# Optimization experiments

Hardware: AMD Instinct MI355X
Metric: run time of the kernel (lower is better)

## Reference

```python
import jax, jax.numpy as jnp
import numpy as np

N, E = 50000, 800000
IN_F, OUT_F, H = 128, 128, 4
D = OUT_F // H  # head dim
NEG_SLOPE = 0.2
EPS = 1e-12


def setup_inputs() -> dict:
    key = jax.random.key(0)
    ks = jax.random.split(key, 10)
    s = 1.0 / np.sqrt(IN_F)
    return {
        "x": jax.random.normal(ks[0], (N, IN_F), jnp.float32),
        "W_src": jax.random.normal(ks[1], (IN_F, H * D), jnp.float32) * s,
        "b_src": jnp.zeros((H * D,), jnp.float32),
        "W_dst": jax.random.normal(ks[2], (IN_F, H * D), jnp.float32) * s,
        "b_dst": jnp.zeros((H * D,), jnp.float32),
        "attn": jax.random.normal(ks[3], (H, D), jnp.float32) * (1.0 / np.sqrt(D)),
        "out_bias": jnp.zeros((H * D,), jnp.float32),
        "ln_w": jnp.ones((OUT_F,), jnp.float32),
        "ln_b": jnp.zeros((OUT_F,), jnp.float32),
        "src": jax.random.randint(ks[4], (E,), 0, N, jnp.int32),
        "dst": jax.random.randint(ks[5], (E,), 0, N, jnp.int32),
    }


def reference(x, W_src, b_src, W_dst, b_dst, attn, out_bias, ln_w, ln_b, src, dst):
    n = x.shape[0]
    # GATv2Conv (share_weights=False): separate source/dest projections
    fs = (x @ W_src + b_src).reshape(n, H, D)  # [N,H,D]
    fd = (x @ W_dst + b_dst).reshape(n, H, D)
    # per-edge scores: e_ij = attn . leaky_relu(fs[u] + fd[v])
    e = jax.nn.leaky_relu(fs[src] + fd[dst], NEG_SLOPE)  # [E,H,D]
    logits = jnp.einsum("ehd,hd->eh", e, attn)  # [E,H]
    # edge softmax over incoming edges of each dst node
    m = jax.ops.segment_max(logits, dst, num_segments=n)  # [N,H]
    ex = jnp.exp(logits - m[dst])
    denom = jax.ops.segment_sum(ex, dst, num_segments=n)  # [N,H]
    alpha = ex / denom[dst]  # [E,H]
    # aggregate: sum_j alpha_ij * fs[j]
    msg = alpha[:, :, None] * fs[src]  # [E,H,D]
    rst = jax.ops.segment_sum(msg, dst, num_segments=n)  # [N,H,D]
    h = rst.reshape(n, H * D) + out_bias
    # LayerNorm (biased variance, eps inside sqrt)
    u = h.mean(-1, keepdims=True)
    s = jnp.mean((h - u) ** 2, -1, keepdims=True)
    h = (h - u) / jnp.sqrt(s + EPS)
    h = ln_w * h + ln_b
    # activation = elu; dropout p=0 -> identity
    return jax.nn.elu(h)
```

## Files before the change

### kernel.cpp

```cpp
#include <hip/hip_runtime.h>
#include <hip/hip_bf16.h>

constexpr int NF = 128;

using bf16x8 = __attribute__((ext_vector_type(8))) short;
using f32x4v = __attribute__((ext_vector_type(4))) float;

__device__ __forceinline__ unsigned short f2bs(float f) {
    return __builtin_bit_cast(unsigned short, __float2bfloat16(f));
}
__device__ __forceinline__ void unpack8(float4 raw, float* a) {
    unsigned u0 = __float_as_uint(raw.x);
    unsigned u1 = __float_as_uint(raw.y);
    unsigned u2 = __float_as_uint(raw.z);
    unsigned u3 = __float_as_uint(raw.w);
    a[0] = __uint_as_float(u0 << 16);
    a[1] = __uint_as_float(u0 & 0xffff0000u);
    a[2] = __uint_as_float(u1 << 16);
    a[3] = __uint_as_float(u1 & 0xffff0000u);
    a[4] = __uint_as_float(u2 << 16);
    a[5] = __uint_as_float(u2 & 0xffff0000u);
    a[6] = __uint_as_float(u3 << 16);
    a[7] = __uint_as_float(u3 & 0xffff0000u);
}

__global__ void GraphAttnLayer_70196945486348_kernel() {}

__global__ __launch_bounds__(256) void prep_kernel(
    const float* __restrict__ Wsrc, const float* __restrict__ Wdst,
    unsigned short* __restrict__ Wb2,
    int* __restrict__ state, int NSB)
{
    int i = blockIdx.x * 256 + threadIdx.x;
    if (i < NSB) state[i] = 0;
    if (i < 16 * 256) {
        int j = i >> 8;
        int t = i & 255;
        int wave = t >> 6;
        int lane = t & 63;
        int lm = lane & 15;
        int kq = (lane >> 4) * 8;
        int c = j >> 2, s = j & 3;
        int col = wave * 64 + c * 16 + lm;
        int ks = s * 32 + kq;
        bf16x8 frag;
#pragma unroll
        for (int m = 0; m < 8; ++m) {
            float v = (col < 128) ? Wsrc[(ks + m) * NF + col]
                                  : Wdst[(ks + m) * NF + (col - 128)];
            frag[m] = (short)f2bs(v);
        }
        *(bf16x8*)(Wb2 + (size_t)i * 8) = frag;
    }
}

__global__ __launch_bounds__(256) void gemm_hist_kernel(
    const float* __restrict__ x,
    const unsigned short* __restrict__ Wb2,
    const float* __restrict__ bsrc, const float* __restrict__ bdst,
    unsigned short* __restrict__ fs,
    float* __restrict__ fd,
    const int* __restrict__ dst,
    int* __restrict__ cntT,
    int N, int E, int C, int B)
{
    __shared__ int lh[256];
    __shared__ float xs[32][129];
    const int t = threadIdx.x;
    if (blockIdx.x < C) {
        lh[t] = 0;
        __syncthreads();
        int e0 = blockIdx.x * 4096;
#pragma unroll
        for (int j = 0; j < 16; ++j) {
            int e = e0 + j * 256 + t;
            if (e < E) atomicAdd(&lh[dst[e] >> 8], 1);
        }
        __syncthreads();
        if (t < B) cntT[t * C + blockIdx.x] = lh[t];
    }

    const int lane = t & 63;
    const int wave = t >> 6;
    const int m_base = blockIdx.x * 32;
    if (m_base >= N) return;
    const int lm = lane & 15;
    const int kq = (lane >> 4) * 8;

    bf16x8 bfrag[4][4];
    float bias[4];
#pragma unroll
    for (int c = 0; c < 4; ++c) {
        int col = wave * 64 + c * 16 + lm;
        bias[c] = (col < 128) ? bsrc[col] : bdst[col - 128];
#pragma unroll
        for (int s = 0; s < 4; ++s)
            bfrag[c][s] = *(const bf16x8*)(Wb2 + ((size_t)((c * 4 + s) * 256 + t)) * 8);
    }

#pragma unroll
    for (int q = 0; q < 4; ++q) {
        int idx = q * 256 + t;
        int row = idx >> 5;
        int c4  = (idx & 31) * 4;
        int grow = m_base + row;
        if (grow >= N) grow = N - 1;
        float4 v = *(const float4*)(x + (size_t)grow * NF + c4);
        xs[row][c4 + 0] = v.x;
        xs[row][c4 + 1] = v.y;
        xs[row][c4 + 2] = v.z;
        xs[row][c4 + 3] = v.w;
    }
    __syncthreads();

    for (int r = 0; r < 2; ++r) {
        int m0 = m_base + r * 16;
        if (m0 >= N) break;
        bf16x8 afrag[4];
#pragma unroll
        for (int s = 0; s < 4; ++s) {
            const float* xp = &xs[r * 16 + lm][s * 32 + kq];
#pragma unroll
            for (int j = 0; j < 8; ++j)
                afrag[s][j] = (short)f2bs(xp[j]);
        }
#pragma unroll
        for (int c = 0; c < 4; ++c) {
            f32x4v acc = {0.f, 0.f, 0.f, 0.f};
#pragma unroll
            for (int s = 0; s < 4; ++s)
                acc = __builtin_amdgcn_mfma_f32_16x16x32_bf16(afrag[s], bfrag[c][s], acc, 0, 0, 0);
            int col = wave * 64 + c * 16 + lm;
            int cc = col & 127;
#pragma unroll
            for (int rr = 0; rr < 4; ++rr) {
                int rowd = m0 + (lane >> 4) * 4 + rr;
                if (rowd < N) {
                    float v = acc[rr] + bias[c];
                    if (col < 128) fs[(size_t)rowd * NF + cc] = f2bs(v);
                    else           fd[(size_t)rowd * NF + cc] = v;
                }
            }
        }
    }
}

__global__ __launch_bounds__(256) void scan_kernel(
    const int* __restrict__ cntT, int* __restrict__ baseBC,
    int* __restrict__ state, int M)
{
    int b = blockIdx.x, t = threadIdx.x;
    int i = b * 256 + t;
    int v = (i < M) ? cntT[i] : 0;

    __shared__ int arr[256];
    __shared__ int s_bofs;
    arr[t] = v;
    __syncthreads();
    for (int off = 1; off < 256; off <<= 1) {
        int u = (t >= off) ? arr[t - off] : 0;
        __syncthreads();
        arr[t] += u;
        __syncthreads();
    }
    int total = arr[255];

    if (t < 64) {
        if (t == 0) {
            int word = ((b == 0 ? 2 : 1) << 30) | total;
            atomicExch(&state[b], word);
        }
        int bofs = 0;
        if (b > 0) {
            int base = b;
            for (;;) {
                int j = base - 1 - t;
                int sv = 0, f = 1;
                if (j >= 0) {
                    sv = __hip_atomic_load(&state[j], __ATOMIC_RELAXED,
                                           __HIP_MEMORY_SCOPE_AGENT);
                    f = ((unsigned)sv) >> 30;
                }
                unsigned long long notready = __ballot(f == 0);
                if (notready) continue;
                unsigned long long has2 = __ballot(f == 2);
                if (has2) {
                    int k = (int)(__ffsll((unsigned long long)has2) - 1);
                    int val = (t <= k) ? (sv & 0x3FFFFFFF) : 0;
#pragma unroll
                    for (int off = 32; off; off >>= 1) val += __shfl_xor(val, off);
                    bofs += val;
                    break;
                } else {
                    int val = (j >= 0) ? (sv & 0x3FFFFFFF) : 0;
#pragma unroll
                    for (int off = 32; off; off >>= 1) val += __shfl_xor(val, off);
                    bofs += val;
                    base -= 64;
                }
            }
            if (t == 0) atomicExch(&state[b], (2 << 30) | (bofs + total));
        }
        if (t == 0) s_bofs = bofs;
    }
    __syncthreads();
    int excl = arr[t] - v + s_bofs;
    if (i < M) baseBC[i] = excl;
}

__global__ __launch_bounds__(256) void scatter_pairs_kernel(
    const int* __restrict__ dst, const int* __restrict__ src,
    const int* __restrict__ baseBC, unsigned* __restrict__ pairs,
    int E, int C, int B)
{
    __shared__ int base_lds[256];
    __shared__ int lcnt[256];
    int chunk = blockIdx.x, t = threadIdx.x;
    if (t < B) base_lds[t] = baseBC[t * C + chunk];
    lcnt[t] = 0;
    __syncthreads();
    int e0 = chunk * 4096;
#pragma unroll
    for (int j = 0; j < 16; ++j) {
        int e = e0 + j * 256 + t;
        if (e < E) {
            int d = dst[e];
            int b = d >> 8;
            int r = atomicAdd(&lcnt[b], 1);
            pairs[base_lds[b] + r] = ((unsigned)(d & 255) << 16) | (unsigned)src[e];
        }
    }
}

__global__ __launch_bounds__(256) void bucket_sort_kernel(
    const unsigned* __restrict__ pairs, const int* __restrict__ baseBC,
    int* __restrict__ rowptr, unsigned short* __restrict__ src_sorted,
    int N, int E, int C, int B)
{
    __shared__ int h[256];
    __shared__ int arr[256];
    __shared__ int cur[256];
    __shared__ unsigned short sorted[16384];
    int b = blockIdx.x, t = threadIdx.x;
    int segbase = baseBC[b * C];
    int end = (b + 1 < B) ? baseBC[(b + 1) * C] : E;
    int count = end - segbase;

    h[t] = 0;
    __syncthreads();
    for (int i = t; i < count; i += 256)
        atomicAdd(&h[pairs[segbase + i] >> 16], 1);
    __syncthreads();
    int v = h[t];
    arr[t] = v;
    __syncthreads();
    for (int off = 1; off < 256; off <<= 1) {
        int u = (t >= off) ? arr[t - off] : 0;
        __syncthreads();
        arr[t] += u;
        __syncthreads();
    }
    int excl = arr[t] - v;
    int node = b * 256 + t;
    if (node <= N) rowptr[node] = segbase + excl;
    cur[t] = excl;
    __syncthreads();
    for (int i = t; i < count; i += 256) {
        unsigned p = pairs[segbase + i];
        int r = atomicAdd(&cur[p >> 16], 1);
        sorted[r] = (unsigned short)(p & 0xFFFF);
    }
    __syncthreads();
    for (int i = t; i < count; i += 256)
        src_sorted[segbase + i] = sorted[i];
}

__global__ __launch_bounds__(256) void node_kernel(
    const float4* __restrict__ fsq,
    const int* __restrict__ rowptr, const unsigned short* __restrict__ src_sorted,
    const float4* __restrict__ attn4,
    const float4* __restrict__ obias4,
    const float4* __restrict__ lnw4,
    const float4* __restrict__ lnb4,
    float4* __restrict__ out4, int N)
{
    int lane = threadIdx.x & 63;
    int es = lane >> 4;
    int g  = lane & 15;
    int n = blockIdx.x * 4 + (threadIdx.x >> 6);
    if (n >= N) return;

    float4 fda = out4[(size_t)n * 32 + g * 2];
    float4 fdb = out4[(size_t)n * 32 + g * 2 + 1];
    float4 ava = attn4[g * 2];
    float4 avb = attn4[g * 2 + 1];
    float fd[8] = {fda.x, fda.y, fda.z, fda.w, fdb.x, fdb.y, fdb.z, fdb.w};
    float av[8] = {ava.x, ava.y, ava.z, ava.w, avb.x, avb.y, avb.z, avb.w};

    int beg = rowptr[n], end = rowptr[n + 1];
    float l = 0.f;
    float ac[8] = {0.f, 0.f, 0.f, 0.f, 0.f, 0.f, 0.f, 0.f};

    for (int j = beg; j < end; j += 4) {
        int idx = j + es;
        bool valid = idx < end;
        int s = src_sorted[valid ? idx : (end - 1)];
        float4 raw = fsq[(size_t)s * 16 + g];
        float a[8];
        unpack8(raw, a);
        float p = 0.f;
#pragma unroll
        for (int d = 0; d < 8; ++d) {
            float t = a[d] + fd[d];
            t = fmaxf(t, 0.2f * t);
            p += av[d] * t;
        }
        p += __shfl_xor(p, 1);
        p += __shfl_xor(p, 2);
        float e = valid ? __expf(p) : 0.f;
        l += e;
#pragma unroll
        for (int d = 0; d < 8; ++d) ac[d] += e * a[d];
    }

    l += __shfl_xor(l, 16);
    l += __shfl_xor(l, 32);
#pragma unroll
    for (int d = 0; d < 8; ++d) {
        ac[d] += __shfl_xor(ac[d], 16);
        ac[d] += __shfl_xor(ac[d], 32);
    }

    float rl = (l > 0.f) ? (1.f / l) : 0.f;
    float4 oba = obias4[g * 2];
    float4 obb = obias4[g * 2 + 1];
    float ob[8] = {oba.x, oba.y, oba.z, oba.w, obb.x, obb.y, obb.z, obb.w};
    float h[8];
    float s1 = 0.f, s2 = 0.f;
#pragma unroll
    for (int d = 0; d < 8; ++d) {
        h[d] = ac[d] * rl + ob[d];
        s1 += h[d];
        s2 += h[d] * h[d];
    }
    s1 += __shfl_xor(s1, 1); s2 += __shfl_xor(s2, 1);
    s1 += __shfl_xor(s1, 2); s2 += __shfl_xor(s2, 2);
    s1 += __shfl_xor(s1, 4); s2 += __shfl_xor(s2, 4);
    s1 += __shfl_xor(s1, 8); s2 += __shfl_xor(s2, 8);

    float u = s1 * (1.f / NF);
    float var = s2 * (1.f / NF) - u * u;
    float rstd = rsqrtf(fmaxf(var, 0.f) + 1e-12f);
    float4 gwa = lnw4[g * 2], gwb = lnw4[g * 2 + 1];
    float4 gba = lnb4[g * 2], gbb = lnb4[g * 2 + 1];
    float gw[8] = {gwa.x, gwa.y, gwa.z, gwa.w, gwb.x, gwb.y, gwb.z, gwb.w};
    float gb[8] = {gba.x, gba.y, gba.z, gba.w, gbb.x, gbb.y, gbb.z, gbb.w};
    float z[8];
#pragma unroll
    for (int d = 0; d < 8; ++d) {
        float y = gw[d] * ((h[d] - u) * rstd) + gb[d];
        z[d] = (y > 0.f) ? y : (__expf(y) - 1.f);
    }
    if (es == 0) {
        out4[(size_t)n * 32 + g * 2]     = make_float4(z[0], z[1], z[2], z[3]);
        out4[(size_t)n * 32 + g * 2 + 1] = make_float4(z[4], z[5], z[6], z[7]);
    }
}

extern "C" void kernel_launch(void* const* d_in, const int* in_sizes, int n_in,
                              void* d_out, int out_size, void* d_ws, size_t ws_size,
                              hipStream_t stream)
{
    const float* x    = (const float*)d_in[0];
    const float* Wsrc = (const float*)d_in[1];
    const float* bsrc = (const float*)d_in[2];
    const float* Wdst = (const float*)d_in[3];
    const float* bdst = (const float*)d_in[4];
    const float4* attn4 = (const float4*)d_in[5];
    const float4* obias4= (const float4*)d_in[6];
    const float4* lnw4  = (const float4*)d_in[7];
    const float4* lnb4  = (const float4*)d_in[8];
    const int* src = (const int*)d_in[9];
    const int* dst = (const int*)d_in[10];
    int N = in_sizes[0] / NF;
    int E = in_sizes[9];

    int C = (E + 4095) / 4096;
    int B = (N + 255) / 256;
    int M = B * C;
    int NSB = (M + 255) / 256;

    int* cntT = (int*)d_ws;
    int* baseBC = cntT + M;
    int* state = baseBC + M;
    int* rowptr = state + 256;
    unsigned* pairs = (unsigned*)(rowptr + (N + 1));
    unsigned short* srcs = (unsigned short*)(pairs + E);
    unsigned short* Wb2 = srcs + ((E + 1) & ~1);
    unsigned short* fs = Wb2 + 16 * 256 * 8;

    int NGB = (N + 31) / 32;
    if (NGB < C) NGB = C;

    prep_kernel<<<B, 256, 0, stream>>>(Wsrc, Wdst, Wb2, state, NSB);
    gemm_hist_kernel<<<NGB, 256, 0, stream>>>(
        x, Wb2, bsrc, bdst, fs, (float*)d_out, dst, cntT, N, E, C, B);
    scan_kernel<<<NSB, 256, 0, stream>>>(cntT, baseBC, state, M);
    scatter_pairs_kernel<<<C, 256, 0, stream>>>(dst, src, baseBC, pairs, E, C, B);
    bucket_sort_kernel<<<B, 256, 0, stream>>>(pairs, baseBC, rowptr, srcs, N, E, C, B);
    node_kernel<<<(N + 3) / 4, 256, 0, stream>>>(
        (const float4*)fs, rowptr, srcs, attn4, obias4, lnw4, lnb4,
        (float4*)d_out, N);
}
```

Baseline: 193.7 us.

## Split projection GEMM across scatter and sort kernels to overlap graph preprocessing

The standalone weight-prep kernel is merged into the histogram kernel, which removes one launch. The projection GEMM tiles are split into two halves that run as extra blocks appended to the scatter-pairs kernel and the bucket-sort kernel. Those edge-sort stages launch few blocks and are latency-bound, so the GEMM work fills otherwise idle CUs. In exchange, the sort kernel's static LDS now includes the GEMM tile buffer on top of the sort buffer, which may lower occupancy for both kinds of block.

```diff
diff --git a/kernel.cpp b/kernel.cpp
--- a/kernel.cpp
+++ b/kernel.cpp
@@ -26,63 +26,18 @@
 
 __global__ void GraphAttnLayer_70196945486348_kernel() {}
 
-__global__ __launch_bounds__(256) void prep_kernel(
-    const float* __restrict__ Wsrc, const float* __restrict__ Wdst,
-    unsigned short* __restrict__ Wb2,
-    int* __restrict__ state, int NSB)
-{
-    int i = blockIdx.x * 256 + threadIdx.x;
-    if (i < NSB) state[i] = 0;
-    if (i < 16 * 256) {
-        int j = i >> 8;
-        int t = i & 255;
-        int wave = t >> 6;
-        int lane = t & 63;
-        int lm = lane & 15;
-        int kq = (lane >> 4) * 8;
-        int c = j >> 2, s = j & 3;
-        int col = wave * 64 + c * 16 + lm;
-        int ks = s * 32 + kq;
-        bf16x8 frag;
-#pragma unroll
-        for (int m = 0; m < 8; ++m) {
-            float v = (col < 128) ? Wsrc[(ks + m) * NF + col]
-                                  : Wdst[(ks + m) * NF + (col - 128)];
-            frag[m] = (short)f2bs(v);
-        }
-        *(bf16x8*)(Wb2 + (size_t)i * 8) = frag;
-    }
-}
-
-__global__ __launch_bounds__(256) void gemm_hist_kernel(
+__device__ __forceinline__ void gemm_tile(
     const float* __restrict__ x,
     const unsigned short* __restrict__ Wb2,
     const float* __restrict__ bsrc, const float* __restrict__ bdst,
-    unsigned short* __restrict__ fs,
-    float* __restrict__ fd,
-    const int* __restrict__ dst,
-    int* __restrict__ cntT,
-    int N, int E, int C, int B)
-{
-    __shared__ int lh[256];
+    unsigned short* __restrict__ fs, float* __restrict__ fd,
+    int tile, int N)
+{
     __shared__ float xs[32][129];
     const int t = threadIdx.x;
-    if (blockIdx.x < C) {
-        lh[t] = 0;
-        __syncthreads();
-        int e0 = blockIdx.x * 4096;
-#pragma unroll
-        for (int j = 0; j < 16; ++j) {
-            int e = e0 + j * 256 + t;
-            if (e < E) atomicAdd(&lh[dst[e] >> 8], 1);
-        }
-        __syncthreads();
-        if (t < B) cntT[t * C + blockIdx.x] = lh[t];
-    }
-
     const int lane = t & 63;
     const int wave = t >> 6;
-    const int m_base = blockIdx.x * 32;
+    const int m_base = tile * 32;
     if (m_base >= N) return;
     const int lm = lane & 15;
     const int kq = (lane >> 4) * 8;
@@ -143,6 +98,50 @@
             }
         }
     }
+}
+
+__global__ __launch_bounds__(256) void hist_prep_kernel(
+    const int* __restrict__ dst,
+    int* __restrict__ cntT,
+    const float* __restrict__ Wsrc, const float* __restrict__ Wdst,
+    unsigned short* __restrict__ Wb2,
+    int* __restrict__ state,
+    int E, int C, int B, int NSB)
+{
+    __shared__ int lh[256];
+    const int t = threadIdx.x;
+    int gi = blockIdx.x * 256 + t;
+    if (gi < NSB) state[gi] = 0;
+    if (gi < 16 * 256) {
+        int j = gi >> 8;
+        int tt = gi & 255;
+        int wave = tt >> 6;
+        int lane = tt & 63;
+        int lm = lane & 15;
+        int kq = (lane >> 4) * 8;
+        int c = j >> 2, s = j & 3;
+        int col = wave * 64 + c * 16 + lm;
+        int ks = s * 32 + kq;
+        bf16x8 frag;
+#pragma unroll
+        for (int m = 0; m < 8; ++m) {
+            float v = (col < 128) ? Wsrc[(ks + m) * NF + col]
+                                  : Wdst[(ks + m) * NF + (col - 128)];
+            frag[m] = (short)f2bs(v);
+        }
+        *(bf16x8*)(Wb2 + (size_t)gi * 8) = frag;
+    }
+
+    lh[t] = 0;
+    __syncthreads();
+    int e0 = blockIdx.x * 4096;
+#pragma unroll
+    for (int j = 0; j < 16; ++j) {
+        int e = e0 + j * 256 + t;
+        if (e < E) atomicAdd(&lh[dst[e] >> 8], 1);
+    }
+    __syncthreads();
+    if (t < B) cntT[t * C + blockIdx.x] = lh[t];
 }
 
 __global__ __launch_bounds__(256) void scan_kernel(
@@ -208,71 +207,87 @@
     if (i < M) baseBC[i] = excl;
 }
 
-__global__ __launch_bounds__(256) void scatter_pairs_kernel(
+__global__ __launch_bounds__(256) void scatter_gemm_kernel(
     const int* __restrict__ dst, const int* __restrict__ src,
     const int* __restrict__ baseBC, unsigned* __restrict__ pairs,
-    int E, int C, int B)
+    const float* __restrict__ x, const unsigned short* __restrict__ Wb2,
+    const float* __restrict__ bsrc, const float* __restrict__ bdst,
+    unsigned short* __restrict__ fs, float* __restrict__ fd,
+    int N, int E, int C, int B)
 {
     __shared__ int base_lds[256];
     __shared__ int lcnt[256];
-    int chunk = blockIdx.x, t = threadIdx.x;
-    if (t < B) base_lds[t] = baseBC[t * C + chunk];
-    lcnt[t] = 0;
-    __syncthreads();
-    int e0 = chunk * 4096;
-#pragma unroll
-    for (int j = 0; j < 16; ++j) {
-        int e = e0 + j * 256 + t;
-        if (e < E) {
-            int d = dst[e];
-            int b = d >> 8;
-            int r = atomicAdd(&lcnt[b], 1);
-            pairs[base_lds[b] + r] = ((unsigned)(d & 255) << 16) | (unsigned)src[e];
-        }
-    }
-}
-
-__global__ __launch_bounds__(256) void bucket_sort_kernel(
+    int t = threadIdx.x;
+    if (blockIdx.x < (unsigned)C) {
+        int chunk = blockIdx.x;
+        if (t < B) base_lds[t] = baseBC[t * C + chunk];
+        lcnt[t] = 0;
+        __syncthreads();
+        int e0 = chunk * 4096;
+#pragma unroll
+        for (int j = 0; j < 16; ++j) {
+            int e = e0 + j * 256 + t;
+            if (e < E) {
+                int d = dst[e];
+                int b = d >> 8;
+                int r = atomicAdd(&lcnt[b], 1);
+                pairs[base_lds[b] + r] = ((unsigned)(d & 255) << 16) | (unsigned)src[e];
+            }
+        }
+    } else {
+        gemm_tile(x, Wb2, bsrc, bdst, fs, fd, blockIdx.x - C, N);
+    }
+}
+
+__global__ __launch_bounds__(256) void sort_gemm_kernel(
     const unsigned* __restrict__ pairs, const int* __restrict__ baseBC,
     int* __restrict__ rowptr, unsigned short* __restrict__ src_sorted,
-    int N, int E, int C, int B)
+    const float* __restrict__ x, const unsigned short* __restrict__ Wb2,
+    const float* __restrict__ bsrc, const float* __restrict__ bdst,
+    unsigned short* __restrict__ fs, float* __restrict__ fd,
+    int N, int E, int C, int B, int T1)
 {
     __shared__ int h[256];
     __shared__ int arr[256];
     __shared__ int cur[256];
     __shared__ unsigned short sorted[16384];
-    int b = blockIdx.x, t = threadIdx.x;
-    int segbase = baseBC[b * C];
-    int end = (b + 1 < B) ? baseBC[(b + 1) * C] : E;
-    int count = end - segbase;
-
-    h[t] = 0;
-    __syncthreads();
-    for (int i = t; i < count; i += 256)
-        atomicAdd(&h[pairs[segbase + i] >> 16], 1);
-    __syncthreads();
-    int v = h[t];
-    arr[t] = v;
-    __syncthreads();
-    for (int off = 1; off < 256; off <<= 1) {
-        int u = (t >= off) ? arr[t - off] : 0;
-        __syncthreads();
-        arr[t] += u;
-        __syncthreads();
-    }
-    int excl = arr[t] - v;
-    int node = b * 256 + t;
-    if (node <= N) rowptr[node] = segbase + excl;
-    cur[t] = excl;
-    __syncthreads();
-    for (int i = t; i < count; i += 256) {
-        unsigned p = pairs[segbase + i];
-        int r = atomicAdd(&cur[p >> 16], 1);
-        sorted[r] = (unsigned short)(p & 0xFFFF);
-    }
-    __syncthreads();
-    for (int i = t; i < count; i += 256)
-        src_sorted[segbase + i] = sorted[i];
+    int t = threadIdx.x;
+    if (blockIdx.x < (unsigned)B) {
+        int b = blockIdx.x;
+        int segbase = baseBC[b * C];
+        int end = (b + 1 < B) ? baseBC[(b + 1) * C] : E;
+        int count = end - segbase;
+
+        h[t] = 0;
+        __syncthreads();
+        for (int i = t; i < count; i += 256)
+            atomicAdd(&h[pairs[segbase + i] >> 16], 1);
+        __syncthreads();
+        int v = h[t];
+        arr[t] = v;
+        __syncthreads();
+        for (int off = 1; off < 256; off <<= 1) {
+            int u = (t >= off) ? arr[t - off] : 0;
+            __syncthreads();
+            arr[t] += u;
+            __syncthreads();
+        }
+        int excl = arr[t] - v;
+        int node = b * 256 + t;
+        if (node <= N) rowptr[node] = segbase + excl;
+        cur[t] = excl;
+        __syncthreads();
+        for (int i = t; i < count; i += 256) {
+            unsigned p = pairs[segbase + i];
+            int r = atomicAdd(&cur[p >> 16], 1);
+            sorted[r] = (unsigned short)(p & 0xFFFF);
+        }
+        __syncthreads();
+        for (int i = t; i < count; i += 256)
+            src_sorted[segbase + i] = sorted[i];
+    } else {
+        gemm_tile(x, Wb2, bsrc, bdst, fs, fd, T1 + (blockIdx.x - B), N);
+    }
 }
 
 __global__ __launch_bounds__(256) void node_kernel(
@@ -389,6 +404,9 @@
     int B = (N + 255) / 256;
     int M = B * C;
     int NSB = (M + 255) / 256;
+    int T = (N + 31) / 32;
+    int T1 = T / 2;
+    int T2 = T - T1;
 
     int* cntT = (int*)d_ws;
     int* baseBC = cntT + M;
@@ -399,15 +417,15 @@
     unsigned short* Wb2 = srcs + ((E + 1) & ~1);
     unsigned short* fs = Wb2 + 16 * 256 * 8;
 
-    int NGB = (N + 31) / 32;
-    if (NGB < C) NGB = C;
-
-    prep_kernel<<<B, 256, 0, stream>>>(Wsrc, Wdst, Wb2, state, NSB);
-    gemm_hist_kernel<<<NGB, 256, 0, stream>>>(
-        x, Wb2, bsrc, bdst, fs, (float*)d_out, dst, cntT, N, E, C, B);
+    hist_prep_kernel<<<C, 256, 0, stream>>>(dst, cntT, Wsrc, Wdst, Wb2,
+                                            state, E, C, B, NSB);
     scan_kernel<<<NSB, 256, 0, stream>>>(cntT, baseBC, state, M);
-    scatter_pairs_kernel<<<C, 256, 0, stream>>>(dst, src, baseBC, pairs, E, C, B);
-    bucket_sort_kernel<<<B, 256, 0, stream>>>(pairs, baseBC, rowptr, srcs, N, E, C, B);
+    scatter_gemm_kernel<<<C + T1, 256, 0, stream>>>(
+        dst, src, baseBC, pairs, x, Wb2, bsrc, bdst, fs, (float*)d_out,
+        N, E, C, B);
+    sort_gemm_kernel<<<B + T2, 256, 0, stream>>>(
+        pairs, baseBC, rowptr, srcs, x, Wb2, bsrc, bdst, fs, (float*)d_out,
+        N, E, C, B, T1);
     node_kernel<<<(N + 3) / 4, 256, 0, stream>>>(
         (const float4*)fs, rowptr, srcs, attn4, obias4, lnw4, lnb4,
         (float4*)d_out, N);
```

Result: faster. 184.6 us (-4.7%).
